# Kernel optimization log

Measured on AMD Instinct MI355X. Metric: run time of the kernel, lower is better.

## Reference

```python
import jax, jax.numpy as jnp
import numpy as np

N_NODES = 100000
N_EDGES = 800000
F_IN = 128
F_OUT = 128
K_HOPS = 2


def setup_inputs() -> dict:
    key = jax.random.key(0)
    k1, k2, k3 = jax.random.split(key, 3)
    x = jax.random.normal(k1, (N_NODES, F_IN), dtype=jnp.float32)
    edge_index = jax.random.randint(k2, (2, N_EDGES), 0, N_NODES, dtype=jnp.int64)
    # SGConv's internal Linear(num_features -> embedding_size), bias=True
    W = jax.random.normal(k3, (F_OUT, F_IN), dtype=jnp.float32) * (1.0 / np.sqrt(F_IN))
    b = jnp.zeros((F_OUT,), dtype=jnp.float32)
    return {"x": x, "W": W, "b": b, "edge_index": edge_index}


def reference(x, W, b, edge_index):
    N = x.shape[0]
    # gcn_norm: add self loops (weight 1), symmetric normalization D^-1/2 (A+I) D^-1/2
    loop = jnp.arange(N, dtype=edge_index.dtype)
    row = jnp.concatenate([edge_index[0], loop])  # source nodes j
    col = jnp.concatenate([edge_index[1], loop])  # target nodes i
    ones = jnp.ones(row.shape[0], dtype=x.dtype)
    deg = jax.ops.segment_sum(ones, col, num_segments=N)
    dinv = jnp.where(deg > 0, jax.lax.rsqrt(deg), jnp.zeros_like(deg))
    norm = dinv[row] * dinv[col]  # [E+N]
    # K-hop propagation: x <- segment_sum(norm * x[row] -> col)
    h = x
    for _ in range(K_HOPS):
        h = jax.ops.segment_sum(norm[:, None] * h[row], col, num_segments=N)
    out = h @ W.T + b  # [N, F_OUT]
    return jax.nn.log_softmax(out, axis=1)
```

## Files before the change

### kernel.cpp

```cpp
#include <hip/hip_runtime.h>
#include <math.h>

#define N_NODES 100000
#define N_EDGES 800000
#define F 128
#define NBUCK ((N_NODES + 255) / 256)
#define NREP 8
#define SCAP_R 512
#define CPAD 32
#define BSPAN 4096

typedef __attribute__((ext_vector_type(8))) short short8;
typedef __attribute__((ext_vector_type(4))) float floatx4;

__device__ __forceinline__ unsigned short f2bf(float f) {
    unsigned u = __float_as_uint(f);
    u += 0x7fffu + ((u >> 16) & 1u);
    return (unsigned short)(u >> 16);
}
__device__ __forceinline__ float bf_lo(unsigned u) { return __uint_as_float(u << 16); }
__device__ __forceinline__ float bf_hi(unsigned u) { return __uint_as_float(u & 0xffff0000u); }
__device__ __forceinline__ unsigned pack2(float a, float b) {
    return (unsigned)f2bf(a) | ((unsigned)f2bf(b) << 16);
}


__global__ void k_fill2(const int* __restrict__ row, const int* __restrict__ col,
                        int* __restrict__ bcnt, unsigned* __restrict__ stage) {
    int e = blockIdx.x * blockDim.x + threadIdx.x;
    if (e >= N_EDGES) return;
    int r = row[e], c = col[e];
    int bk = c >> 8;
    int ctr = (bk << 3) | (blockIdx.x & (NREP - 1));
    int p = atomicAdd(&bcnt[ctr * CPAD], 1);
    if (p < SCAP_R)
        stage[(size_t)ctr * SCAP_R + p] = ((unsigned)(c & 255) << 20) | (unsigned)(r + 1);
}


__global__ __launch_bounds__(256) void k_build(const int* __restrict__ bcnt,
                                               const unsigned* __restrict__ stage,
                                               unsigned* __restrict__ csr,
                                               int2* __restrict__ rp2,
                                               float* __restrict__ dinv,
                                               float* __restrict__ dinv2) {
    __shared__ int hist[256];
    __shared__ int sc[256];
    __shared__ int cursor[256];
    __shared__ int spanTot;
    __shared__ unsigned img[BSPAN];
    int bk = blockIdx.x, t = threadIdx.x;
    hist[t] = 0;
    __syncthreads();
#pragma unroll
    for (int rep = 0; rep < NREP; ++rep) {
        int ctr = (bk << 3) | rep;
        int n = bcnt[ctr * CPAD]; n = n < SCAP_R ? n : SCAP_R;
        const unsigned* sp = stage + (size_t)ctr * SCAP_R;
        for (int i = t; i < n; i += 256) atomicAdd(&hist[sp[i] >> 20], 1);
    }
    __syncthreads();
    int cdeg = hist[t];
    int pad = (cdeg + 7) & ~7;
    sc[t] = pad;
    __syncthreads();
#pragma unroll
    for (int off = 1; off < 256; off <<= 1) {
        int u = (t >= off) ? sc[t - off] : 0;
        __syncthreads();
        sc[t] += u;
        __syncthreads();
    }
    int excl = sc[t] - pad;
    if (t == 255) spanTot = sc[255];
    cursor[t] = excl;
    __syncthreads();
    int tot = spanTot;
    int node = bk * 256 + t;
    if (node < N_NODES) {
        int base = bk * BSPAN;
        rp2[node] = (int2){base + excl, base + excl + pad};
        float d = rsqrtf((float)cdeg + 1.0f);
        dinv[node] = d; dinv2[node] = d * d;
    }
    for (int i = t; i < tot; i += 256) img[i] = 0u;
    __syncthreads();
#pragma unroll
    for (int rep = 0; rep < NREP; ++rep) {
        int ctr = (bk << 3) | rep;
        int n = bcnt[ctr * CPAD]; n = n < SCAP_R ? n : SCAP_R;
        const unsigned* sp = stage + (size_t)ctr * SCAP_R;
        for (int i = t; i < n; i += 256) {
            unsigned v = sp[i];
            int pos = atomicAdd(&cursor[v >> 20], 1);
            img[pos] = v & 0xFFFFFu;
        }
    }
    __syncthreads();
    unsigned* op = csr + (size_t)bk * BSPAN;
    for (int i = t; i < tot; i += 256) op[i] = img[i];
}

__global__ void k_prep(const float4* __restrict__ x, const float* __restrict__ dinv,
                       uint2* __restrict__ xb, uint2* __restrict__ h1b) {
    int i = blockIdx.x * blockDim.x + threadIdx.x;
    if (i < 32) { xb[i] = (uint2){0u, 0u}; h1b[i] = (uint2){0u, 0u}; }
    if (i >= N_NODES * 32) return;
    int node = i >> 5;
    float d = dinv[node];
    float4 v = x[i];
    uint2 o; o.x = pack2(d * v.x, d * v.y); o.y = pack2(d * v.z, d * v.w);
    xb[i + 32] = o;
}


__global__ __launch_bounds__(256) void k_hop(const int2* __restrict__ rp2,
                                             const unsigned* __restrict__ csr,
                                             const float* __restrict__ scale,
                                             const uint2* __restrict__ src,
                                             uint2* __restrict__ dst) {
    int wv = (blockIdx.x * blockDim.x + threadIdx.x) >> 6;
    int lane = threadIdx.x & 63;
    int half = lane >> 5, off = lane & 31;
    int node = wv * 2 + half;
    if (node >= N_NODES) return;
    uint2 u = src[(size_t)(node + 1) * 32 + off];
    float a0 = bf_lo(u.x), a1 = bf_hi(u.x);
    float a2 = bf_lo(u.y), a3 = bf_hi(u.y);
    int2 rp = rp2[node];
    int e = rp.x, end = rp.y;
    for (; e < end; e += 8) {
        const uint4* cp = (const uint4*)(csr + e);
        uint4 c0 = cp[0], c1 = cp[1];
        unsigned idx[8] = {c0.x, c0.y, c0.z, c0.w, c1.x, c1.y, c1.z, c1.w};
#pragma unroll
        for (int j = 0; j < 8; ++j) {
            uint2 v = src[(size_t)idx[j] * 32 + off];
            a0 += bf_lo(v.x); a1 += bf_hi(v.x);
            a2 += bf_lo(v.y); a3 += bf_hi(v.y);
        }
    }
    float s = scale[node];
    uint2 o; o.x = pack2(s * a0, s * a1); o.y = pack2(s * a2, s * a3);
    dst[(size_t)(node + 1) * 32 + off] = o;
}


__global__ __launch_bounds__(256) void k_gemm_lsm_mfma(const unsigned short* __restrict__ h,
                                                       const float* __restrict__ W,
                                                       const float* __restrict__ b,
                                                       float* __restrict__ out) {
    int lane = threadIdx.x & 63;
    int wave = threadIdx.x >> 6;
    int m = lane & 15, quad = lane >> 4;

    short8 bfr[8][4];
    float bv[8];
#pragma unroll
    for (int t = 0; t < 8; ++t) {
        bv[t] = b[16 * t + m];
        const float* wr = W + (size_t)(16 * t + m) * 128;
#pragma unroll
        for (int ks = 0; ks < 4; ++ks) {
            const float* wp = wr + ks * 32 + quad * 8;
            short8 v;
#pragma unroll
            for (int j = 0; j < 8; ++j) v[j] = (short)f2bf(wp[j]);
            bfr[t][ks] = v;
        }
    }

    const int ngroups = (N_NODES + 63) / 64;
    for (int g = blockIdx.x; g < ngroups; g += gridDim.x) {
        int gbase = g * 64 + wave * 16;
        int nodeA = gbase + m;
        int node_c = nodeA < N_NODES ? nodeA : N_NODES - 1;
        short8 a[4];
#pragma unroll
        for (int ks = 0; ks < 4; ++ks)
            a[ks] = *(const short8*)(h + (size_t)node_c * 128 + ks * 32 + quad * 8);
        floatx4 acc[8];
#pragma unroll
        for (int t = 0; t < 8; ++t) acc[t] = (floatx4){bv[t], bv[t], bv[t], bv[t]};
#pragma unroll
        for (int ks = 0; ks < 4; ++ks)
#pragma unroll
            for (int t = 0; t < 8; ++t)
                acc[t] = __builtin_amdgcn_mfma_f32_16x16x32_bf16(a[ks], bfr[t][ks], acc[t], 0, 0, 0);

#pragma unroll
        for (int r = 0; r < 4; ++r) {
            float mx = acc[0][r];
#pragma unroll
            for (int t = 1; t < 8; ++t) mx = fmaxf(mx, acc[t][r]);
#pragma unroll
            for (int msk = 1; msk < 16; msk <<= 1) mx = fmaxf(mx, __shfl_xor(mx, msk));
            float sm = 0.f;
#pragma unroll
            for (int t = 0; t < 8; ++t) sm += __expf(acc[t][r] - mx);
#pragma unroll
            for (int msk = 1; msk < 16; msk <<= 1) sm += __shfl_xor(sm, msk);
            float l = mx + __logf(sm);
            int rown = gbase + quad * 4 + r;
            if (rown < N_NODES) {
                float* op = out + (size_t)rown * 128 + m;
#pragma unroll
                for (int t = 0; t < 8; ++t) op[16 * t] = acc[t][r] - l;
            }
        }
    }
}


extern "C" void kernel_launch(void* const* d_in, const int* in_sizes, int n_in,
                              void* d_out, int out_size, void* d_ws, size_t ws_size,
                              hipStream_t stream) {
    const float* x = (const float*)d_in[0];
    const float* W = (const float*)d_in[1];
    const float* b = (const float*)d_in[2];
    const int* edge = (const int*)d_in[3];
    const int* row = edge;
    const int* col = edge + N_EDGES;
    float* out = (float*)d_out;

    int*      bcnt  = (int*)d_ws;
    float*    dinv  = (float*)(bcnt + NBUCK * NREP * CPAD + 256);
    float*    dinv2 = dinv + 102400;
    int2*     rp2   = (int2*)(dinv2 + 102400);
    unsigned* csr   = (unsigned*)(rp2 + 102400);
    uint2*    xb    = (uint2*)(csr + (size_t)NBUCK * BSPAN);
    uint2*    h1b   = xb + 32 * (N_NODES + 1);
    uint2*    h2b   = xb;
    unsigned* stage = (unsigned*)(h1b + 32);

    int nb_edges = (N_EDGES + 255) / 256;
    int nb_prep = (N_NODES * 32 + 255) / 256;

    hipMemsetAsync(bcnt, 0, (size_t)NBUCK * NREP * CPAD * 4, stream);
    k_fill2<<<nb_edges, 256, 0, stream>>>(row, col, bcnt, stage);
    k_build<<<NBUCK, 256, 0, stream>>>(bcnt, stage, csr, rp2, dinv, dinv2);
    k_prep<<<nb_prep, 256, 0, stream>>>((const float4*)x, dinv, xb, h1b);

    int hop_blocks = (N_NODES / 2 * 64) / 256;
    k_hop<<<hop_blocks, 256, 0, stream>>>(rp2, csr, dinv2, xb, h1b);
    k_hop<<<hop_blocks, 256, 0, stream>>>(rp2, csr, dinv, h1b, h2b);

    k_gemm_lsm_mfma<<<512, 256, 0, stream>>>((const unsigned short*)(h2b + 32), W, b, out);
}
```

Measured before the change: 261.5 us.

## Stage bf16 weights in swizzled LDS instead of registers in GEMM+log-softmax kernel

The GEMM/log-softmax kernel no longer keeps the whole 128x128 bf16 weight matrix in per-thread registers (32 short8 values). Each block now converts W to bf16 once into a 32KB shared-memory tile using an XOR swizzle to avoid bank conflicts, and the MFMA loop reads B fragments from LDS. Launch bounds of 4 blocks per SM and a grid of 1024 blocks aim to raise occupancy and hide the latency of the global loads of h. The cost is extra LDS reads inside the inner loop and a per-block weight conversion.

```diff
diff --git a/kernel.cpp b/kernel.cpp
--- a/kernel.cpp
+++ b/kernel.cpp
@@ -146,29 +146,29 @@
 }
 
 
-__global__ __launch_bounds__(256) void k_gemm_lsm_mfma(const unsigned short* __restrict__ h,
-                                                       const float* __restrict__ W,
-                                                       const float* __restrict__ b,
-                                                       float* __restrict__ out) {
-    int lane = threadIdx.x & 63;
-    int wave = threadIdx.x >> 6;
+__global__ __launch_bounds__(256, 4) void k_gemm_lsm_mfma(const unsigned short* __restrict__ h,
+                                                          const float4* __restrict__ W4,
+                                                          const float* __restrict__ b,
+                                                          float* __restrict__ out) {
+    __shared__ unsigned short wlds[128 * 128];
+    int tid = threadIdx.x;
+    int lane = tid & 63;
+    int wave = tid >> 6;
     int m = lane & 15, quad = lane >> 4;
 
-    short8 bfr[8][4];
+#pragma unroll
+    for (int it = 0; it < 16; ++it) {
+        int i = tid + it * 256;
+        int row = i >> 5, col4 = i & 31;
+        float4 v = W4[i];
+        uint2 o; o.x = pack2(v.x, v.y); o.y = pack2(v.z, v.w);
+        unsigned byte = ((unsigned)(row * 256 + col4 * 8)) ^ (((unsigned)row & 7u) << 4);
+        *(uint2*)((char*)wlds + byte) = o;
+    }
     float bv[8];
 #pragma unroll
-    for (int t = 0; t < 8; ++t) {
-        bv[t] = b[16 * t + m];
-        const float* wr = W + (size_t)(16 * t + m) * 128;
-#pragma unroll
-        for (int ks = 0; ks < 4; ++ks) {
-            const float* wp = wr + ks * 32 + quad * 8;
-            short8 v;
-#pragma unroll
-            for (int j = 0; j < 8; ++j) v[j] = (short)f2bf(wp[j]);
-            bfr[t][ks] = v;
-        }
-    }
+    for (int t = 0; t < 8; ++t) bv[t] = b[16 * t + m];
+    __syncthreads();
 
     const int ngroups = (N_NODES + 63) / 64;
     for (int g = blockIdx.x; g < ngroups; g += gridDim.x) {
@@ -183,10 +183,15 @@
 #pragma unroll
         for (int t = 0; t < 8; ++t) acc[t] = (floatx4){bv[t], bv[t], bv[t], bv[t]};
 #pragma unroll
-        for (int ks = 0; ks < 4; ++ks)
-#pragma unroll
-            for (int t = 0; t < 8; ++t)
-                acc[t] = __builtin_amdgcn_mfma_f32_16x16x32_bf16(a[ks], bfr[t][ks], acc[t], 0, 0, 0);
+        for (int t = 0; t < 8; ++t) {
+#pragma unroll
+            for (int ks = 0; ks < 4; ++ks) {
+                unsigned byte = ((unsigned)((16 * t + m) * 256 + ks * 64 + quad * 16))
+                              ^ (((unsigned)m & 7u) << 4);
+                short8 bf = *(const short8*)((const char*)wlds + byte);
+                acc[t] = __builtin_amdgcn_mfma_f32_16x16x32_bf16(a[ks], bf, acc[t], 0, 0, 0);
+            }
+        }
 
 #pragma unroll
         for (int r = 0; r < 4; ++r) {
@@ -245,5 +250,6 @@
     k_hop<<<hop_blocks, 256, 0, stream>>>(rp2, csr, dinv2, xb, h1b);
     k_hop<<<hop_blocks, 256, 0, stream>>>(rp2, csr, dinv, h1b, h2b);
 
-    k_gemm_lsm_mfma<<<512, 256, 0, stream>>>((const unsigned short*)(h2b + 32), W, b, out);
-}
+    k_gemm_lsm_mfma<<<1024, 256, 0, stream>>>((const unsigned short*)(h2b + 32),
+                                              (const float4*)W, b, out);
+}
```

New measurement: 287.7 us. 10.0% more time.
